# Kernel optimization log

Hardware: AMD Instinct MI355X
Metric: run time of the kernel (lower is better)

The kernel has to match this reference:

```python
import jax, jax.numpy as jnp
import numpy as np
from jax import lax

HEADS = 4
DIM = 64
GATE_HID = 16


def setup_inputs() -> dict:
    key = jax.random.key(0)
    ks = jax.random.split(key, 12)
    b, c, h, w = 2, DIM, 48, 48
    s = 0.05
    x = jax.random.normal(ks[0], (b, c, h, w), jnp.float32)
    Wqkv = jax.random.normal(ks[1], (3 * c, c), jnp.float32) * s
    bqkv = jax.random.normal(ks[2], (3 * c,), jnp.float32) * s
    Wpos = jax.random.normal(ks[3], (3 * c, 1, 3, 3), jnp.float32) * s
    bpos = jax.random.normal(ks[4], (3 * c,), jnp.float32) * s
    Wg1 = jax.random.normal(ks[5], (GATE_HID, 1), jnp.float32) * 0.5
    bg1 = jax.random.normal(ks[6], (GATE_HID,), jnp.float32) * 0.1
    Wg2 = jax.random.normal(ks[7], (1, GATE_HID), jnp.float32) * 0.5
    bg2 = jax.random.normal(ks[8], (1,), jnp.float32) * 0.1
    Wproj = jax.random.normal(ks[9], (c, c), jnp.float32) * s
    bproj = jax.random.normal(ks[10], (c,), jnp.float32) * s
    return {"x": x, "Wqkv": Wqkv, "bqkv": bqkv, "Wpos": Wpos, "bpos": bpos,
            "Wg1": Wg1, "bg1": bg1, "Wg2": Wg2, "bg2": bg2,
            "Wproj": Wproj, "bproj": bproj}


def _forward(x, Wqkv, bqkv, Wpos, bpos, Wg1, bg1, Wg2, bg2, Wproj, bproj):
    b, c, h, w = x.shape
    n = h * w
    heads = HEADS
    hd = c // heads
    scale = hd ** -0.5
    # qkv 1x1 conv then 3x3 depthwise positional conv
    qkv = jnp.einsum('bchw,oc->bohw', x, Wqkv) + bqkv[None, :, None, None]
    qkv = lax.conv_general_dilated(
        qkv, Wpos, window_strides=(1, 1), padding='SAME',
        feature_group_count=3 * c,
        dimension_numbers=('NCHW', 'OIHW', 'NCHW')) + bpos[None, :, None, None]
    q, k, v = jnp.split(qkv, 3, axis=1)

    def to_heads(t):
        # [b,c,h,w] -> [b,heads,n,hd]
        return t.reshape(b, c, n).transpose(0, 2, 1).reshape(b, n, heads, hd).transpose(0, 2, 1, 3)

    q, k, v = to_heads(q), to_heads(k), to_heads(v)
    attn = jnp.einsum('bhid,bhjd->bhij', q, k) * scale  # [b,heads,n,n]
    prob = jax.nn.softmax(attn, axis=-1)
    entropy = -(prob * jnp.log(jnp.clip(prob, 1e-12))).sum(-1).mean(-1)  # [b,heads]
    # entropy gate: sigmoid(fc2(relu(fc1(e)))) * 0.9 + 0.1
    hgate = jax.nn.relu(entropy[..., None] @ Wg1.T + bg1)  # [b,heads,16]
    ratio = jax.nn.sigmoid(hgate @ Wg2.T + bg2)[..., 0] * 0.9 + 0.1  # [b,heads]
    # dynamic per-(batch,head) top-k along rows via rank threshold
    keep = jnp.clip(jnp.ceil(ratio * n).astype(jnp.int32), 1, n)  # [b,heads]
    sorted_desc = -jnp.sort(-attn, axis=-1)  # [b,heads,n,n]
    idx = jnp.broadcast_to((keep - 1)[:, :, None, None], (b, heads, n, 1))
    thresh = jnp.take_along_axis(sorted_desc, idx, axis=-1)  # [b,heads,n,1]
    sparse = jnp.where(attn >= thresh, attn, -jnp.inf)
    p = jax.nn.softmax(sparse, axis=-1)
    out = jnp.einsum('bhij,bhjd->bhid', p, v)  # [b,heads,n,hd]
    out = out.transpose(0, 2, 1, 3).reshape(b, n, c)
    out = out @ Wproj.T + bproj
    return out.transpose(0, 2, 1).reshape(b, c, h, w)


def reference(x, Wqkv, bqkv, Wpos, bpos, Wg1, bg1, Wg2, bg2, Wproj, bproj):
    return _forward(x, Wqkv, bqkv, Wpos, bpos, Wg1, bg1, Wg2, bg2, Wproj, bproj)
```

## Files before the change

### kernel.cpp

```cpp
#include <hip/hip_runtime.h>
#include <hip/hip_fp16.h>


#define NEG_INF (-__builtin_huge_valf())

typedef _Float16 half8_t __attribute__((ext_vector_type(8)));
typedef float floatx4 __attribute__((ext_vector_type(4)));

__device__ __forceinline__ unsigned h2key(unsigned short u) {
  return (u & 0x8000u) ? (unsigned)((~u) & 0xFFFFu) : (unsigned)(u | 0x8000u);
}
__device__ __forceinline__ float key16_to_float(unsigned k) {
  unsigned short u = (k & 0x8000u) ? (unsigned short)(k & 0x7FFFu)
                                   : (unsigned short)((~k) & 0xFFFFu);
  return __half2float(__ushort_as_half(u));
}

__device__ __forceinline__ float max8(uint4 v, float mx) {
  float2 f0 = __half22float2(*(__half2*)&v.x);
  float2 f1 = __half22float2(*(__half2*)&v.y);
  float2 f2 = __half22float2(*(__half2*)&v.z);
  float2 f3 = __half22float2(*(__half2*)&v.w);
  mx = fmaxf(mx, fmaxf(fmaxf(f0.x, f0.y), fmaxf(f1.x, f1.y)));
  mx = fmaxf(mx, fmaxf(fmaxf(f2.x, f2.y), fmaxf(f3.x, f3.y)));
  return mx;
}

__device__ __forceinline__ uint4 maskExp8(uint4 v, float th, float m,
                                          float& sp) {
  float2 f0 = __half22float2(*(__half2*)&v.x);
  float2 f1 = __half22float2(*(__half2*)&v.y);
  float2 f2 = __half22float2(*(__half2*)&v.z);
  float2 f3 = __half22float2(*(__half2*)&v.w);
  float p0 = (f0.x >= th) ? __expf(f0.x - m) : 0.f;
  float p1 = (f0.y >= th) ? __expf(f0.y - m) : 0.f;
  float p2 = (f1.x >= th) ? __expf(f1.x - m) : 0.f;
  float p3 = (f1.y >= th) ? __expf(f1.y - m) : 0.f;
  float p4 = (f2.x >= th) ? __expf(f2.x - m) : 0.f;
  float p5 = (f2.y >= th) ? __expf(f2.y - m) : 0.f;
  float p6 = (f3.x >= th) ? __expf(f3.x - m) : 0.f;
  float p7 = (f3.y >= th) ? __expf(f3.y - m) : 0.f;
  sp += ((p0 + p1) + (p2 + p3)) + ((p4 + p5) + (p6 + p7));
  uint4 o;
  __half2 h0 = __floats2half2_rn(p0, p1); o.x = *(unsigned*)&h0;
  __half2 h1 = __floats2half2_rn(p2, p3); o.y = *(unsigned*)&h1;
  __half2 h2 = __floats2half2_rn(p4, p5); o.z = *(unsigned*)&h2;
  __half2 h3 = __floats2half2_rn(p6, p7); o.w = *(unsigned*)&h3;
  return o;
}

__global__ __launch_bounds__(256) void k_qkv(const float* __restrict__ x,
                                             const float* __restrict__ W,
                                             const float* __restrict__ bias,
                                             float* __restrict__ out,
                                             float* __restrict__ ent) {
  if (blockIdx.x == 0 && threadIdx.x < 8) ent[threadIdx.x] = 0.f;
  int blk = blockIdx.x;
  int chunk = blk % 9;
  int og = (blk / 9) % 48;
  int b = blk / (9 * 48);
  int o0 = og * 4;
  int pos = chunk * 256 + threadIdx.x;
  const float* xb = x + b * 64 * 2304 + pos;
  const float* w0 = W + (o0 + 0) * 64;
  const float* w1 = W + (o0 + 1) * 64;
  const float* w2 = W + (o0 + 2) * 64;
  const float* w3 = W + (o0 + 3) * 64;
  float a0 = bias[o0 + 0], a1 = bias[o0 + 1];
  float a2 = bias[o0 + 2], a3 = bias[o0 + 3];
#pragma unroll
  for (int c = 0; c < 64; c++) {
    float xv = xb[c * 2304];
    a0 = fmaf(w0[c], xv, a0);
    a1 = fmaf(w1[c], xv, a1);
    a2 = fmaf(w2[c], xv, a2);
    a3 = fmaf(w3[c], xv, a3);
  }
  out[(b * 192 + o0 + 0) * 2304 + pos] = a0;
  out[(b * 192 + o0 + 1) * 2304 + pos] = a1;
  out[(b * 192 + o0 + 2) * 2304 + pos] = a2;
  out[(b * 192 + o0 + 3) * 2304 + pos] = a3;
}

__global__ __launch_bounds__(256) void k_dw(const float* __restrict__ qkv,
                                            const float* __restrict__ Wpos,
                                            const float* __restrict__ bpos,
                                            _Float16* __restrict__ q2,
                                            _Float16* __restrict__ k2,
                                            _Float16* __restrict__ vt) {
  __shared__ float smem[16][384];
  int blk = blockIdx.x;
  int chunk = blk % 9;
  int sel = (blk / 9) % 3;
  int head = (blk / 27) % 4;
  int b = blk / 108;
  int chbase = sel * 64 + head * 16;
  int bh = b * 4 + head;
  int tid = threadIdx.x;
  int p0 = chunk * 256;
  int baserow = p0 / 48;
  int rA = min(max(baserow - 1, 0), 40);

  const float* src = qkv + (size_t)(b * 192 + chbase) * 2304;
#pragma unroll
  for (int l = 0; l < 24; l++) {
    int idx = tid + l * 256;
    int ch = idx / 384;
    int off = idx - ch * 384;
    int rr = off / 48;
    int cc = off - rr * 48;
    smem[ch][off] = src[(size_t)ch * 2304 + (rA + rr) * 48 + cc];
  }
  __syncthreads();

  int pos = p0 + tid;
  int yy = pos / 48, xx = pos - yy * 48;
  int ry = yy - rA;
  float accv[16];
#pragma unroll
  for (int d = 0; d < 16; d++) {
    const float* w = Wpos + (chbase + d) * 9;
    float a = bpos[chbase + d];
#pragma unroll
    for (int dy = -1; dy <= 1; dy++) {
      int y2 = yy + dy;
      if ((unsigned)y2 < 48u) {
#pragma unroll
        for (int dx = -1; dx <= 1; dx++) {
          int x2 = xx + dx;
          if ((unsigned)x2 < 48u)
            a = fmaf(w[(dy + 1) * 3 + (dx + 1)], smem[d][(ry + dy) * 48 + x2],
                     a);
        }
      }
    }
    accv[d] = a;
  }

  if (sel == 2) {
#pragma unroll
    for (int d = 0; d < 16; d++)
      vt[((size_t)bh * 16 + d) * 2304 + pos] = (_Float16)accv[d];
  } else {
    _Float16 h1[16], h2[16];
#pragma unroll
    for (int d = 0; d < 16; d++) {
      float a = (sel == 0) ? accv[d] * 0.25f : accv[d];
      h1[d] = (_Float16)a;
      h2[d] = (_Float16)(a - (float)h1[d]);
    }
    _Float16* dst = ((sel == 0) ? q2 : k2) + ((size_t)bh * 2304 + pos) * 32;
    uint4* d4 = (uint4*)dst;
    d4[0] = *(uint4*)&h1[0];
    d4[1] = *(uint4*)&h1[8];
    d4[2] = *(uint4*)&h2[0];
    d4[3] = *(uint4*)&h2[8];
  }
}

template <bool STORE>
__global__ __launch_bounds__(256) void k_ent_t(const _Float16* __restrict__ q2,
                                               const _Float16* __restrict__ k2,
                                               float* __restrict__ ent,
                                               _Float16* __restrict__ lgH) {
  __shared__ __align__(16) _Float16 tBuf[4][16][72];
  __shared__ float mWv[4][16];
  __shared__ float mFin[16];
  __shared__ float sWv[4][16], uWv[4][16];

  int blk = blockIdx.x;
  int rowtile = blk % 144;
  int bh = blk / 144;
  int row0 = rowtile * 16;
  int tid = threadIdx.x, lane = tid & 63, wave = tid >> 6;
  int m16 = lane & 15, quad = lane >> 4;

  const half8_t* q2v =
      (const half8_t*)(q2 + ((size_t)bh * 2304 + row0 + m16) * 32);
  half8_t A1 = q2v[quad];
  half8_t zh = {};
  half8_t A2 = (lane < 32) ? A1 : zh;
  const half8_t* kbase = (const half8_t*)(k2 + (size_t)bh * 2304 * 32);

  float mreg[4] = {NEG_INF, NEG_INF, NEG_INF, NEG_INF};
  for (int g = 0; g < 9; g++) {
#pragma unroll
    for (int tt = 0; tt < 4; tt++) {
      int t = g * 4 + tt;
      int col = wave * 576 + t * 16 + m16;
      const half8_t* kk = kbase + (size_t)col * 4;
      half8_t b1 = kk[quad & 1];
      half8_t b2 = kk[2 + (quad & 1)];
      floatx4 acc = {};
      acc = __builtin_amdgcn_mfma_f32_16x16x32_f16(A2, b2, acc, 0, 0, 0);
      acc = __builtin_amdgcn_mfma_f32_16x16x32_f16(A1, b1, acc, 0, 0, 0);
#pragma unroll
      for (int i = 0; i < 4; i++) {
        mreg[i] = fmaxf(mreg[i], acc[i]);
        if (STORE) tBuf[wave][quad * 4 + i][tt * 16 + m16] = (_Float16)acc[i];
      }
    }
    if (STORE) {
      __syncthreads();
      int rb = lane >> 3, seg = lane & 7;
#pragma unroll
      for (int it = 0; it < 2; it++) {
        int rr = it * 8 + rb;
        uint4 vv = *(const uint4*)&tBuf[wave][rr][seg * 8];
        *(uint4*)(lgH + ((size_t)bh * 2304 + row0 + rr) * 2304 + wave * 576 +
                  g * 64 + seg * 8) = vv;
      }
      __syncthreads();
    }
  }
#pragma unroll
  for (int off = 1; off < 16; off <<= 1)
#pragma unroll
    for (int i = 0; i < 4; i++)
      mreg[i] = fmaxf(mreg[i], __shfl_xor(mreg[i], off));
  if (m16 == 0) {
#pragma unroll
    for (int i = 0; i < 4; i++) mWv[wave][quad * 4 + i] = mreg[i];
  }
  __syncthreads();
  if (tid < 16) {
    mFin[tid] = fmaxf(fmaxf(mWv[0][tid], mWv[1][tid]),
                      fmaxf(mWv[2][tid], mWv[3][tid]));
  }
  __syncthreads();

  float mrow[4];
#pragma unroll
  for (int i = 0; i < 4; i++) mrow[i] = mFin[quad * 4 + i];
  float s[4] = {0.f, 0.f, 0.f, 0.f}, u[4] = {0.f, 0.f, 0.f, 0.f};
#pragma unroll 4
  for (int t = 0; t < 36; t++) {
    int col = wave * 576 + t * 16 + m16;
    const half8_t* kk = kbase + (size_t)col * 4;
    half8_t b1 = kk[quad & 1];
    half8_t b2 = kk[2 + (quad & 1)];
    floatx4 acc = {};
    acc = __builtin_amdgcn_mfma_f32_16x16x32_f16(A2, b2, acc, 0, 0, 0);
    acc = __builtin_amdgcn_mfma_f32_16x16x32_f16(A1, b1, acc, 0, 0, 0);
#pragma unroll
    for (int i = 0; i < 4; i++) {
      float z = acc[i] - mrow[i];
      float e = __expf(z);
      s[i] += e;
      u[i] = fmaf(z, e, u[i]);
    }
  }
#pragma unroll
  for (int off = 1; off < 16; off <<= 1) {
#pragma unroll
    for (int i = 0; i < 4; i++) {
      s[i] += __shfl_xor(s[i], off);
      u[i] += __shfl_xor(u[i], off);
    }
  }
  if (m16 == 0) {
#pragma unroll
    for (int i = 0; i < 4; i++) {
      sWv[wave][quad * 4 + i] = s[i];
      uWv[wave][quad * 4 + i] = u[i];
    }
  }
  __syncthreads();
  if (tid < 16) {
    float S = sWv[0][tid] + sWv[1][tid] + sWv[2][tid] + sWv[3][tid];
    float U = uWv[0][tid] + uWv[1][tid] + uWv[2][tid] + uWv[3][tid];
    float er = __logf(S) - U / S;
    er += __shfl_xor(er, 1);
    er += __shfl_xor(er, 2);
    er += __shfl_xor(er, 4);
    er += __shfl_xor(er, 8);
    if (tid == 0) atomicAdd(&ent[bh], er);
  }
}

template <bool CACHED>
__global__ __launch_bounds__(256, 7) void k_attn_t(
    const _Float16* __restrict__ q2, const _Float16* __restrict__ k2,
    const _Float16* __restrict__ vt, const _Float16* __restrict__ lgH,
    const float* __restrict__ ent, const float* __restrict__ Wg1,
    const float* __restrict__ bg1, const float* __restrict__ Wg2,
    const float* __restrict__ bg2, float* __restrict__ oh) {
  __shared__ __align__(16) _Float16 pbuf[4][2320];
  __shared__ float sS[4];
  __shared__ float mShF[4][4];
  __shared__ __align__(16) float redSh[4][64];

  int blk = blockIdx.x;
  int rowblk = blk % 576;
  int bh = blk / 576;
  int row0 = rowblk * 4;
  int tid = threadIdx.x, lane = tid & 63, wave = tid >> 6;

  float eAvg = ent[bh] * (1.f / 2304.f);
  float gacc = bg2[0];
#pragma unroll
  for (int i = 0; i < 16; i++) {
    float h = fmaxf(fmaf(eAvg, Wg1[i], bg1[i]), 0.f);
    gacc = fmaf(h, Wg2[i], gacc);
  }
  float ratio = 0.9f / (1.f + __expf(-gacc)) + 0.1f;
  int kp = (int)ceilf(ratio * 2304.f);
  unsigned keep = (unsigned)min(max(kp, 1), 2304);

  float m;
  uint4* dst4 = (uint4*)pbuf[wave];
  if (CACHED) {
    const uint4* src =
        (const uint4*)(lgH + ((size_t)bh * 2304 + row0 + wave) * 2304);
    float mx = NEG_INF;
#pragma unroll
    for (int it = 0; it < 4; it++) {
      int idx = lane + it * 64;
      uint4 v = src[idx];
      dst4[idx] = v;
      mx = max8(v, mx);
    }
    if (lane < 32) {
      uint4 v = src[256 + lane];
      dst4[256 + lane] = v;
      mx = max8(v, mx);
    }
#pragma unroll
    for (int off = 1; off < 64; off <<= 1) mx = fmaxf(mx, __shfl_xor(mx, off));
    m = mx;
  } else {
    int m16 = lane & 15, quad = lane >> 4;
    const half8_t* q2v =
        (const half8_t*)(q2 + ((size_t)bh * 2304 + row0 + (m16 & 3)) * 32);
    half8_t A1 = q2v[quad];
    half8_t zh = {};
    half8_t A2 = (lane < 32) ? A1 : zh;
    const half8_t* kbase = (const half8_t*)(k2 + (size_t)bh * 2304 * 32);
    float ml[4] = {NEG_INF, NEG_INF, NEG_INF, NEG_INF};
#pragma unroll 4
    for (int t = 0; t < 36; t++) {
      int ct = wave * 36 + t;
      int col = ct * 16 + m16;
      const half8_t* kk = kbase + (size_t)col * 4;
      half8_t b1 = kk[quad & 1];
      half8_t b2 = kk[2 + (quad & 1)];
      floatx4 acc = {};
      acc = __builtin_amdgcn_mfma_f32_16x16x32_f16(A2, b2, acc, 0, 0, 0);
      acc = __builtin_amdgcn_mfma_f32_16x16x32_f16(A1, b1, acc, 0, 0, 0);
      if (lane < 16) {
#pragma unroll
        for (int i = 0; i < 4; i++) {
          pbuf[i][ct * 16 + lane] = (_Float16)acc[i];
          ml[i] = fmaxf(ml[i], acc[i]);
        }
      }
    }
#pragma unroll
    for (int off = 1; off < 16; off <<= 1)
#pragma unroll
      for (int i = 0; i < 4; i++) ml[i] = fmaxf(ml[i], __shfl_xor(ml[i], off));
    if (lane == 0) {
#pragma unroll
      for (int i = 0; i < 4; i++) mShF[wave][i] = ml[i];
    }
    __syncthreads();
    m = fmaxf(fmaxf(mShF[0][wave], mShF[1][wave]),
              fmaxf(mShF[2][wave], mShF[3][wave]));
  }

  float th;
  {
    const unsigned short* prow = (const unsigned short*)pbuf[wave];
    unsigned keys[36];
#pragma unroll
    for (int i = 0; i < 36; i++) keys[i] = h2key(prow[lane + i * 64]);
    unsigned T = 0u;
    for (int bit = 15; bit >= 0; --bit) {
      unsigned cand = T | (1u << bit);
      unsigned cnt = 0u;
#pragma unroll
      for (int i = 0; i < 36; i++)
        cnt += (unsigned)__popcll(__ballot(keys[i] >= cand));
      if (cnt >= keep) {
        T = cand;
        if (cnt == keep) break;
      }
    }
    th = key16_to_float(T);
  }

  {
    float sp = 0.f;
#pragma unroll
    for (int it = 0; it < 4; it++) {
      int idx = lane + it * 64;
      dst4[idx] = maskExp8(dst4[idx], th, m, sp);
    }
    if (lane < 32) {
      int idx = 256 + lane;
      dst4[idx] = maskExp8(dst4[idx], th, m, sp);
    }
#pragma unroll
    for (int off = 1; off < 64; off <<= 1) sp += __shfl_xor(sp, off);
    if (lane == 0) sS[wave] = sp;
  }
  __syncthreads();

  {
    int m16 = lane & 15, quad = lane >> 4;
    const _Float16* vrow = vt + ((size_t)bh * 16 + m16) * 2304;
    const _Float16* prow = pbuf[m16 & 3];
    int jb0 = wave * 576 + quad * 8;
    floatx4 acc = {};
#pragma unroll 6
    for (int t = 0; t < 18; t++) {
      int jb = jb0 + t * 32;
      half8_t a = *(const half8_t*)&prow[jb];
      half8_t b = *(const half8_t*)&vrow[jb];
      acc = __builtin_amdgcn_mfma_f32_16x16x32_f16(a, b, acc, 0, 0, 0);
    }
    if (lane < 16) {
      *(floatx4*)&redSh[wave][m16 * 4] = acc;
    }
  }
  __syncthreads();
  if (tid < 64) {
    int r = tid & 3, d = tid >> 2;
    float s2 = redSh[0][d * 4 + r] + redSh[1][d * 4 + r] +
               redSh[2][d * 4 + r] + redSh[3][d * 4 + r];
    oh[((size_t)(bh * 2304 + row0 + r)) * 16 + d] = s2 / sS[r];
  }
}

__global__ __launch_bounds__(256) void k_proj(const float* __restrict__ oh,
                                              const float* __restrict__ Wp,
                                              const float* __restrict__ bp,
                                              float* __restrict__ out) {
  int blk = blockIdx.x;
  int chunk = blk % 9;
  int cog = (blk / 9) % 16;
  int b = blk / (9 * 16);
  int co0 = cog * 4;
  int pos = chunk * 256 + threadIdx.x;
  float a0 = bp[co0 + 0], a1 = bp[co0 + 1], a2 = bp[co0 + 2], a3 = bp[co0 + 3];
#pragma unroll
  for (int head = 0; head < 4; head++) {
    const float4* op =
        (const float4*)(oh + ((size_t)((b * 4 + head) * 2304 + pos)) * 16);
#pragma unroll
    for (int p = 0; p < 4; p++) {
      float4 o4 = op[p];
#pragma unroll
      for (int i = 0; i < 4; i++) {
        const float* wr = Wp + (co0 + i) * 64 + head * 16 + p * 4;
        float* ai = (i == 0) ? &a0 : ((i == 1) ? &a1 : ((i == 2) ? &a2 : &a3));
        *ai = fmaf(wr[0], o4.x, *ai);
        *ai = fmaf(wr[1], o4.y, *ai);
        *ai = fmaf(wr[2], o4.z, *ai);
        *ai = fmaf(wr[3], o4.w, *ai);
      }
    }
  }
  out[(b * 64 + co0 + 0) * 2304 + pos] = a0;
  out[(b * 64 + co0 + 1) * 2304 + pos] = a1;
  out[(b * 64 + co0 + 2) * 2304 + pos] = a2;
  out[(b * 64 + co0 + 3) * 2304 + pos] = a3;
}

extern "C" void kernel_launch(void* const* d_in, const int* in_sizes, int n_in,
                              void* d_out, int out_size, void* d_ws,
                              size_t ws_size, hipStream_t stream) {
  const float* x    = (const float*)d_in[0];
  const float* Wqkv = (const float*)d_in[1];
  const float* bqkv = (const float*)d_in[2];
  const float* Wpos = (const float*)d_in[3];
  const float* bpos = (const float*)d_in[4];
  const float* Wg1  = (const float*)d_in[5];
  const float* bg1  = (const float*)d_in[6];
  const float* Wg2  = (const float*)d_in[7];
  const float* bg2  = (const float*)d_in[8];
  const float* Wpr  = (const float*)d_in[9];
  const float* bpr  = (const float*)d_in[10];
  float* out = (float*)d_out;

  const size_t lgBytes = (size_t)8 * 2304 * 2304 * 2;
  const size_t baseBytes = (size_t)(884736 + 294912 + 8) * 4 +
                           (size_t)(2 * 589824 + 294912) * 2;
  bool cached = ws_size >= lgBytes + baseBytes;

  char* base = (char*)d_ws;
  _Float16* lgH = nullptr;
  if (cached) {
    lgH = (_Float16*)base;
    base += lgBytes;
  }
  float* qkv_raw = (float*)base;
  float* oh = qkv_raw + 884736;
  float* ent = oh + 294912;
  _Float16* q2 = (_Float16*)(ent + 8);
  _Float16* k2 = q2 + 589824;
  _Float16* vt = k2 + 589824;

  hipLaunchKernelGGL(k_qkv, dim3(2 * 48 * 9), dim3(256), 0, stream,
                     x, Wqkv, bqkv, qkv_raw, ent);
  hipLaunchKernelGGL(k_dw, dim3(216), dim3(256), 0, stream,
                     qkv_raw, Wpos, bpos, q2, k2, vt);
  if (cached) {
    hipLaunchKernelGGL((k_ent_t<true>), dim3(8 * 144), dim3(256), 0, stream,
                       q2, k2, ent, lgH);
    hipLaunchKernelGGL((k_attn_t<true>), dim3(8 * 576), dim3(256), 0, stream,
                       q2, k2, vt, lgH, ent, Wg1, bg1, Wg2, bg2, oh);
  } else {
    hipLaunchKernelGGL((k_ent_t<false>), dim3(8 * 144), dim3(256), 0, stream,
                       q2, k2, ent, lgH);
    hipLaunchKernelGGL((k_attn_t<false>), dim3(8 * 576), dim3(256), 0, stream,
                       q2, k2, vt, lgH, ent, Wg1, bg1, Wg2, bg2, oh);
  }
  hipLaunchKernelGGL(k_proj, dim3(2 * 16 * 9), dim3(256), 0, stream,
                     oh, Wpr, bpr, out);
}
```

Measured before the change: 209.1 us.

## Fuse qkv projection into depthwise conv, keep attention rows in registers, remap blocks

The separate 1x1 qkv projection kernel is removed. The depthwise conv kernel now computes the projection for its halo tile directly into shared memory, which drops one launch and the fp32 qkv round trip, at the cost of recomputing halo rows and running a heavier per-thread FMA loop on only 216 blocks. In the attention kernel each lane keeps its row logits as 36 floats in registers in a new strided layout. The radix threshold search then compares floats instead of re-reading shared memory keys, and the block-index mapping is permuted, probably to improve cache locality. Register pressure rises under the 7-blocks-per-CU launch bound.

```diff
diff --git a/kernel.cpp b/kernel.cpp
--- a/kernel.cpp
+++ b/kernel.cpp
@@ -16,79 +16,26 @@
   return __half2float(__ushort_as_half(u));
 }
 
-__device__ __forceinline__ float max8(uint4 v, float mx) {
+__device__ __forceinline__ void unpack8(uint4 v, float* o) {
   float2 f0 = __half22float2(*(__half2*)&v.x);
   float2 f1 = __half22float2(*(__half2*)&v.y);
   float2 f2 = __half22float2(*(__half2*)&v.z);
   float2 f3 = __half22float2(*(__half2*)&v.w);
-  mx = fmaxf(mx, fmaxf(fmaxf(f0.x, f0.y), fmaxf(f1.x, f1.y)));
-  mx = fmaxf(mx, fmaxf(fmaxf(f2.x, f2.y), fmaxf(f3.x, f3.y)));
-  return mx;
-}
-
-__device__ __forceinline__ uint4 maskExp8(uint4 v, float th, float m,
-                                          float& sp) {
-  float2 f0 = __half22float2(*(__half2*)&v.x);
-  float2 f1 = __half22float2(*(__half2*)&v.y);
-  float2 f2 = __half22float2(*(__half2*)&v.z);
-  float2 f3 = __half22float2(*(__half2*)&v.w);
-  float p0 = (f0.x >= th) ? __expf(f0.x - m) : 0.f;
-  float p1 = (f0.y >= th) ? __expf(f0.y - m) : 0.f;
-  float p2 = (f1.x >= th) ? __expf(f1.x - m) : 0.f;
-  float p3 = (f1.y >= th) ? __expf(f1.y - m) : 0.f;
-  float p4 = (f2.x >= th) ? __expf(f2.x - m) : 0.f;
-  float p5 = (f2.y >= th) ? __expf(f2.y - m) : 0.f;
-  float p6 = (f3.x >= th) ? __expf(f3.x - m) : 0.f;
-  float p7 = (f3.y >= th) ? __expf(f3.y - m) : 0.f;
-  sp += ((p0 + p1) + (p2 + p3)) + ((p4 + p5) + (p6 + p7));
-  uint4 o;
-  __half2 h0 = __floats2half2_rn(p0, p1); o.x = *(unsigned*)&h0;
-  __half2 h1 = __floats2half2_rn(p2, p3); o.y = *(unsigned*)&h1;
-  __half2 h2 = __floats2half2_rn(p4, p5); o.z = *(unsigned*)&h2;
-  __half2 h3 = __floats2half2_rn(p6, p7); o.w = *(unsigned*)&h3;
-  return o;
-}
-
-__global__ __launch_bounds__(256) void k_qkv(const float* __restrict__ x,
-                                             const float* __restrict__ W,
-                                             const float* __restrict__ bias,
-                                             float* __restrict__ out,
-                                             float* __restrict__ ent) {
-  if (blockIdx.x == 0 && threadIdx.x < 8) ent[threadIdx.x] = 0.f;
-  int blk = blockIdx.x;
-  int chunk = blk % 9;
-  int og = (blk / 9) % 48;
-  int b = blk / (9 * 48);
-  int o0 = og * 4;
-  int pos = chunk * 256 + threadIdx.x;
-  const float* xb = x + b * 64 * 2304 + pos;
-  const float* w0 = W + (o0 + 0) * 64;
-  const float* w1 = W + (o0 + 1) * 64;
-  const float* w2 = W + (o0 + 2) * 64;
-  const float* w3 = W + (o0 + 3) * 64;
-  float a0 = bias[o0 + 0], a1 = bias[o0 + 1];
-  float a2 = bias[o0 + 2], a3 = bias[o0 + 3];
-#pragma unroll
-  for (int c = 0; c < 64; c++) {
-    float xv = xb[c * 2304];
-    a0 = fmaf(w0[c], xv, a0);
-    a1 = fmaf(w1[c], xv, a1);
-    a2 = fmaf(w2[c], xv, a2);
-    a3 = fmaf(w3[c], xv, a3);
-  }
-  out[(b * 192 + o0 + 0) * 2304 + pos] = a0;
-  out[(b * 192 + o0 + 1) * 2304 + pos] = a1;
-  out[(b * 192 + o0 + 2) * 2304 + pos] = a2;
-  out[(b * 192 + o0 + 3) * 2304 + pos] = a3;
-}
-
-__global__ __launch_bounds__(256) void k_dw(const float* __restrict__ qkv,
+  o[0] = f0.x; o[1] = f0.y; o[2] = f1.x; o[3] = f1.y;
+  o[4] = f2.x; o[5] = f2.y; o[6] = f3.x; o[7] = f3.y;
+}
+
+__global__ __launch_bounds__(256) void k_dw(const float* __restrict__ x,
+                                            const float* __restrict__ Wqkv,
+                                            const float* __restrict__ bqkv,
                                             const float* __restrict__ Wpos,
                                             const float* __restrict__ bpos,
                                             _Float16* __restrict__ q2,
                                             _Float16* __restrict__ k2,
-                                            _Float16* __restrict__ vt) {
+                                            _Float16* __restrict__ vt,
+                                            float* __restrict__ ent) {
   __shared__ float smem[16][384];
+  if (blockIdx.x == 0 && threadIdx.x < 8) ent[threadIdx.x] = 0.f;
   int blk = blockIdx.x;
   int chunk = blk % 9;
   int sel = (blk / 9) % 3;
@@ -101,15 +48,24 @@
   int baserow = p0 / 48;
   int rA = min(max(baserow - 1, 0), 40);
 
-  const float* src = qkv + (size_t)(b * 192 + chbase) * 2304;
-#pragma unroll
-  for (int l = 0; l < 24; l++) {
-    int idx = tid + l * 256;
-    int ch = idx / 384;
-    int off = idx - ch * 384;
-    int rr = off / 48;
-    int cc = off - rr * 48;
-    smem[ch][off] = src[(size_t)ch * 2304 + (rA + rr) * 48 + cc];
+  for (int rep = 0; rep < 2; rep++) {
+    int pw = tid + rep * 256;
+    if (pw < 384) {
+      int gpos = rA * 48 + pw;
+      const float* xb = x + b * 64 * 2304 + gpos;
+      float acc[16];
+#pragma unroll
+      for (int d = 0; d < 16; d++) acc[d] = bqkv[chbase + d];
+#pragma unroll 8
+      for (int c = 0; c < 64; c++) {
+        float xv = xb[c * 2304];
+#pragma unroll
+        for (int d = 0; d < 16; d++)
+          acc[d] = fmaf(Wqkv[(chbase + d) * 64 + c], xv, acc[d]);
+      }
+#pragma unroll
+      for (int d = 0; d < 16; d++) smem[d][pw] = acc[d];
+    }
   }
   __syncthreads();
 
@@ -290,9 +246,14 @@
   __shared__ float mShF[4][4];
   __shared__ __align__(16) float redSh[4][64];
 
-  int blk = blockIdx.x;
-  int rowblk = blk % 576;
-  int bh = blk / 576;
+  int a = blockIdx.x;
+  int v8 = a & 7;
+  int idx = a >> 3;
+  int q = idx & 3;
+  int pi = idx >> 2;
+  int bh = pi / 18;
+  int rowtile = v8 + (pi % 18) * 8;
+  int rowblk = rowtile * 4 + q;
   int row0 = rowblk * 4;
   int tid = threadIdx.x, lane = tid & 63, wave = tid >> 6;
 
@@ -307,24 +268,25 @@
   int kp = (int)ceilf(ratio * 2304.f);
   unsigned keep = (unsigned)min(max(kp, 1), 2304);
 
+  float v[36];
   float m;
-  uint4* dst4 = (uint4*)pbuf[wave];
   if (CACHED) {
-    const uint4* src =
-        (const uint4*)(lgH + ((size_t)bh * 2304 + row0 + wave) * 2304);
+    const _Float16* src = lgH + ((size_t)bh * 2304 + row0 + wave) * 2304;
+    const uint4* s4 = (const uint4*)src;
     float mx = NEG_INF;
 #pragma unroll
     for (int it = 0; it < 4; it++) {
-      int idx = lane + it * 64;
-      uint4 v = src[idx];
-      dst4[idx] = v;
-      mx = max8(v, mx);
-    }
-    if (lane < 32) {
-      uint4 v = src[256 + lane];
-      dst4[256 + lane] = v;
-      mx = max8(v, mx);
-    }
+      uint4 r = s4[lane + it * 64];
+      unpack8(r, &v[it * 8]);
+    }
+    {
+      uint2 r2 = *(const uint2*)(src + 2048 + lane * 4);
+      float2 f0 = __half22float2(*(__half2*)&r2.x);
+      float2 f1 = __half22float2(*(__half2*)&r2.y);
+      v[32] = f0.x; v[33] = f0.y; v[34] = f1.x; v[35] = f1.y;
+    }
+#pragma unroll
+    for (int i = 0; i < 36; i++) mx = fmaxf(mx, v[i]);
 #pragma unroll
     for (int off = 1; off < 64; off <<= 1) mx = fmaxf(mx, __shfl_xor(mx, off));
     m = mx;
@@ -366,21 +328,26 @@
     __syncthreads();
     m = fmaxf(fmaxf(mShF[0][wave], mShF[1][wave]),
               fmaxf(mShF[2][wave], mShF[3][wave]));
+    const _Float16* src = pbuf[wave];
+    const uint4* s4 = (const uint4*)src;
+#pragma unroll
+    for (int it = 0; it < 4; it++) unpack8(s4[lane + it * 64], &v[it * 8]);
+    uint2 r2 = *(const uint2*)(src + 2048 + lane * 4);
+    float2 f0 = __half22float2(*(__half2*)&r2.x);
+    float2 f1 = __half22float2(*(__half2*)&r2.y);
+    v[32] = f0.x; v[33] = f0.y; v[34] = f1.x; v[35] = f1.y;
   }
 
   float th;
   {
-    const unsigned short* prow = (const unsigned short*)pbuf[wave];
-    unsigned keys[36];
-#pragma unroll
-    for (int i = 0; i < 36; i++) keys[i] = h2key(prow[lane + i * 64]);
     unsigned T = 0u;
     for (int bit = 15; bit >= 0; --bit) {
       unsigned cand = T | (1u << bit);
+      float cf = key16_to_float(cand);
       unsigned cnt = 0u;
 #pragma unroll
       for (int i = 0; i < 36; i++)
-        cnt += (unsigned)__popcll(__ballot(keys[i] >= cand));
+        cnt += (unsigned)__popcll(__ballot(v[i] >= cf));
       if (cnt >= keep) {
         T = cand;
         if (cnt == keep) break;
@@ -391,14 +358,33 @@
 
   {
     float sp = 0.f;
+    uint4* prow4 = (uint4*)pbuf[wave];
 #pragma unroll
     for (int it = 0; it < 4; it++) {
-      int idx = lane + it * 64;
-      dst4[idx] = maskExp8(dst4[idx], th, m, sp);
-    }
-    if (lane < 32) {
-      int idx = 256 + lane;
-      dst4[idx] = maskExp8(dst4[idx], th, m, sp);
+      float p[8];
+#pragma unroll
+      for (int e = 0; e < 8; e++) {
+        float av = v[it * 8 + e];
+        p[e] = (av >= th) ? __expf(av - m) : 0.f;
+        sp += p[e];
+      }
+      uint4 o;
+      __half2 h0 = __floats2half2_rn(p[0], p[1]); o.x = *(unsigned*)&h0;
+      __half2 h1 = __floats2half2_rn(p[2], p[3]); o.y = *(unsigned*)&h1;
+      __half2 h2 = __floats2half2_rn(p[4], p[5]); o.z = *(unsigned*)&h2;
+      __half2 h3 = __floats2half2_rn(p[6], p[7]); o.w = *(unsigned*)&h3;
+      prow4[lane + it * 64] = o;
+    }
+    {
+      float p0 = (v[32] >= th) ? __expf(v[32] - m) : 0.f;
+      float p1 = (v[33] >= th) ? __expf(v[33] - m) : 0.f;
+      float p2 = (v[34] >= th) ? __expf(v[34] - m) : 0.f;
+      float p3 = (v[35] >= th) ? __expf(v[35] - m) : 0.f;
+      sp += (p0 + p1) + (p2 + p3);
+      uint2 o;
+      __half2 h0 = __floats2half2_rn(p0, p1); o.x = *(unsigned*)&h0;
+      __half2 h1 = __floats2half2_rn(p2, p3); o.y = *(unsigned*)&h1;
+      *(uint2*)(pbuf[wave] + 2048 + lane * 4) = o;
     }
 #pragma unroll
     for (int off = 1; off < 64; off <<= 1) sp += __shfl_xor(sp, off);
@@ -415,9 +401,9 @@
 #pragma unroll 6
     for (int t = 0; t < 18; t++) {
       int jb = jb0 + t * 32;
-      half8_t a = *(const half8_t*)&prow[jb];
-      half8_t b = *(const half8_t*)&vrow[jb];
-      acc = __builtin_amdgcn_mfma_f32_16x16x32_f16(a, b, acc, 0, 0, 0);
+      half8_t a2 = *(const half8_t*)&prow[jb];
+      half8_t b2 = *(const half8_t*)&vrow[jb];
+      acc = __builtin_amdgcn_mfma_f32_16x16x32_f16(a2, b2, acc, 0, 0, 0);
     }
     if (lane < 16) {
       *(floatx4*)&redSh[wave][m16 * 4] = acc;
@@ -484,8 +470,8 @@
   float* out = (float*)d_out;
 
   const size_t lgBytes = (size_t)8 * 2304 * 2304 * 2;
-  const size_t baseBytes = (size_t)(884736 + 294912 + 8) * 4 +
-                           (size_t)(2 * 589824 + 294912) * 2;
+  const size_t baseBytes =
+      (size_t)(294912 + 8) * 4 + (size_t)(2 * 589824 + 294912) * 2;
   bool cached = ws_size >= lgBytes + baseBytes;
 
   char* base = (char*)d_ws;
@@ -494,17 +480,14 @@
     lgH = (_Float16*)base;
     base += lgBytes;
   }
-  float* qkv_raw = (float*)base;
-  float* oh = qkv_raw + 884736;
+  float* oh = (float*)base;
   float* ent = oh + 294912;
   _Float16* q2 = (_Float16*)(ent + 8);
   _Float16* k2 = q2 + 589824;
   _Float16* vt = k2 + 589824;
 
-  hipLaunchKernelGGL(k_qkv, dim3(2 * 48 * 9), dim3(256), 0, stream,
-                     x, Wqkv, bqkv, qkv_raw, ent);
   hipLaunchKernelGGL(k_dw, dim3(216), dim3(256), 0, stream,
-                     qkv_raw, Wpos, bpos, q2, k2, vt);
+                     x, Wqkv, bqkv, Wpos, bpos, q2, k2, vt, ent);
   if (cached) {
     hipLaunchKernelGGL((k_ent_t<true>), dim3(8 * 144), dim3(256), 0, stream,
                        q2, k2, ent, lgH);
```

After: 218.3 us. +4.4%, slower.
